# Kernel optimization log

Hardware: AMD Instinct MI355X
Metric: run time of the kernel (lower is better)

Reference implementation:

```python
import jax, jax.numpy as jnp
import numpy as np

IN_F = 2048
OUT_F = 2048
BS = 64  # block_size
NIB = IN_F // BS   # 32 in-blocks
NOB = OUT_F // BS  # 32 out-blocks


def setup_inputs() -> dict:
    key = jax.random.key(0)
    k_x, k_s1, k_s2, k_m = jax.random.split(key, 4)
    bound = 1.0 / np.sqrt(BS)
    x = jax.random.normal(k_x, (4, 4096, IN_F), dtype=jnp.float32)
    stage1 = jax.random.uniform(k_s1, (NIB * BS, BS), minval=-bound, maxval=bound, dtype=jnp.float32)
    stage2 = jax.random.uniform(k_s2, (NOB * BS, BS), minval=-bound, maxval=bound, dtype=jnp.float32)
    mix_w = jax.random.normal(k_m, (NOB * BS, NIB * BS), dtype=jnp.float32) / np.sqrt(IN_F)
    return {"x": x, "stage1": stage1, "stage2": stage2, "mix_w": mix_w}


def _blockdiag(x, weight, num_blocks):
    # x: [..., num_blocks*BS]; weight: [num_blocks*BS, BS] viewed as [g, c, d]
    shape = x.shape[:-1]
    xg = x.reshape(-1, num_blocks, BS)
    w = weight.reshape(num_blocks, BS, BS)
    y = jnp.einsum('ngc,gcd->ngd', xg, w)
    return y.reshape(*shape, num_blocks * BS)


def _shuffle(x):
    # interpret last dim as [BS, NIB], transpose to [NIB, BS]
    shape = x.shape[:-1]
    return x.reshape(-1, BS, NIB).transpose(0, 2, 1).reshape(*shape, NIB * BS)


def reference(x, stage1, stage2, mix_w):
    h = _blockdiag(x, stage1, NIB)          # [B,S,IN_F]
    h = _shuffle(h)                          # [B,S,IN_F]
    h = jnp.einsum('bsi,oi->bso', h, mix_w)  # dense mix, no bias
    return _blockdiag(h, stage2, NOB)        # [B,S,OUT_F]
```

## Files before the change

kernel.cpp:

```cpp
#include <hip/hip_runtime.h>
#include <stdint.h>

#define IN_F 2048
#define OUT_F 2048
#define MTOK 16384

typedef __attribute__((ext_vector_type(8))) __bf16 bf16x8;
typedef __attribute__((ext_vector_type(4))) float f32x4;
typedef __attribute__((ext_vector_type(4))) unsigned short us4;
typedef __attribute__((ext_vector_type(8))) unsigned short us8;

typedef const __attribute__((address_space(1))) void g_void;
typedef __attribute__((address_space(3))) void l_void;

__device__ __forceinline__ void async16(void* lds, const void* g) {
    __builtin_amdgcn_global_load_lds((g_void*)(uintptr_t)g, (l_void*)(uintptr_t)lds, 16, 0, 0);
}

__device__ __forceinline__ unsigned short f2bf(float x) {
    union { float f; uint32_t u; } v; v.f = x;
    uint32_t r = v.u + 0x7fffu + ((v.u >> 16) & 1u);
    return (unsigned short)(r >> 16);
}

__global__ void k_permute_mixw(const float* __restrict__ W, unsigned short* __restrict__ Bp) {
    __shared__ float row[2112];
    const int t = threadIdx.x;
    const float* src = W + (size_t)blockIdx.x * IN_F;
#pragma unroll
    for (int q = 0; q < 2; ++q) {
        int id4 = q * 256 + t;
        float4 v = *(const float4*)(src + id4 * 4);
        int i = id4 * 4;
        int b = i + (i >> 5);
        row[b] = v.x; row[b + 1] = v.y; row[b + 2] = v.z; row[b + 3] = v.w;
    }
    __syncthreads();
    unsigned short* dst = Bp + (size_t)blockIdx.x * IN_F;
#pragma unroll
    for (int q = 0; q < 8; ++q) {
        int j = q * 256 + t;
        int i = ((j & 31) << 6) | (j >> 5);
        dst[j] = f2bf(row[i + (i >> 5)]);
    }
}

__global__ void k_transpose_stages(const float* __restrict__ s1, const float* __restrict__ s2,
                                   unsigned short* __restrict__ W1T, unsigned short* __restrict__ W2T) {
    __shared__ float tile[64 * 65];
    const int b = blockIdx.x;
    const float* src = (b < 32 ? s1 : s2) + (size_t)(b & 31) * 4096;
    unsigned short* dst = (b < 32 ? W1T : W2T) + (size_t)(b & 31) * 4096;
    const int t = threadIdx.x;
#pragma unroll
    for (int q = 0; q < 16; ++q) {
        int id = q * 256 + t;
        tile[(id >> 6) * 65 + (id & 63)] = src[id];
    }
    __syncthreads();
#pragma unroll
    for (int q = 0; q < 16; ++q) {
        int id = q * 256 + t;
        int d = id >> 6, c = id & 63;
        dst[id] = f2bf(tile[c * 65 + d]);
    }
}

#define XS_LD 72
__global__ __launch_bounds__(256, 2) void k_stage1(
    const float* __restrict__ X, const unsigned short* __restrict__ W1T,
    unsigned short* __restrict__ H) {
    __shared__ unsigned short Xs[128 * XS_LD];
    __shared__ unsigned short Ws[64 * XS_LD];
    const int t = threadIdx.x;
    const int lane = t & 63, wave = t >> 6;
    const int quad = lane >> 4, l16 = lane & 15;
    const int m0 = blockIdx.x * 128;
    const int g = blockIdx.y;

    const unsigned short* Wg = W1T + g * 4096;
#pragma unroll
    for (int p = 0; p < 2; ++p) {
        int id = p * 256 + t;
        int r = id >> 3, c = id & 7;
        us8 v = *(const us8*)(Wg + r * 64 + c * 8);
        *(us8*)(Ws + r * XS_LD + c * 8) = v;
    }

    const float* Xg = X + (size_t)m0 * IN_F + g * 64;
#pragma unroll
    for (int q = 0; q < 8; ++q) {
        int id = q * 256 + t;
        int r = id >> 4, c4 = id & 15;
        float4 v = *(const float4*)(Xg + (size_t)r * IN_F + c4 * 4);
        us4 b; b.x = f2bf(v.x); b.y = f2bf(v.y); b.z = f2bf(v.z); b.w = f2bf(v.w);
        *(us4*)(Xs + r * XS_LD + c4 * 4) = b;
    }
    __syncthreads();

    f32x4 acc[2][4];
#pragma unroll
    for (int i = 0; i < 2; ++i)
#pragma unroll
        for (int j = 0; j < 4; ++j) acc[i][j] = (f32x4)0.f;

#pragma unroll
    for (int ks = 0; ks < 2; ++ks) {
        bf16x8 af[2], bfr[4];
#pragma unroll
        for (int i = 0; i < 2; ++i)
            af[i] = *(const bf16x8*)(Xs + (wave * 32 + i * 16 + l16) * XS_LD + ks * 32 + quad * 8);
#pragma unroll
        for (int j = 0; j < 4; ++j)
            bfr[j] = *(const bf16x8*)(Ws + (j * 16 + l16) * XS_LD + ks * 32 + quad * 8);
#pragma unroll
        for (int i = 0; i < 2; ++i)
#pragma unroll
            for (int j = 0; j < 4; ++j)
                acc[i][j] = __builtin_amdgcn_mfma_f32_16x16x32_bf16(af[i], bfr[j], acc[i][j], 0, 0, 0);
    }

    __syncthreads();
    unsigned short* Hs = Xs;
#pragma unroll
    for (int i = 0; i < 2; ++i)
#pragma unroll
        for (int j = 0; j < 4; ++j)
#pragma unroll
            for (int r = 0; r < 4; ++r)
                Hs[(wave * 32 + i * 16 + quad * 4 + r) * 64 + j * 16 + l16] = f2bf(acc[i][j][r]);
    __syncthreads();
#pragma unroll
    for (int p = 0; p < 4; ++p) {
        int id = p * 256 + t;
        int r = id >> 3, c = id & 7;
        us8 v = *(const us8*)(Hs + r * 64 + c * 8);
        *(us8*)(H + (size_t)(m0 + r) * IN_F + g * 64 + c * 8) = v;
    }
}

__global__ __launch_bounds__(256, 2) void k_mix_gemm(
    const unsigned short* __restrict__ A, const unsigned short* __restrict__ B,
    const unsigned short* __restrict__ W2T, float* __restrict__ C) {
    __shared__ unsigned short smem[16384];
    unsigned short* As = smem;
    unsigned short* Bs = smem + 8192;
    const int t = threadIdx.x;
    const int lane = t & 63, wave = t >> 6;
    const int quad = lane >> 4, l16 = lane & 15;
    const int mw = wave & 1, nw = wave >> 1;
    const int m0 = blockIdx.x * 128;
    const int n0 = blockIdx.y * 128;
    const int rr = t >> 3, chunk = t & 7;
    const int gsw = (chunk ^ (rr & 7)) * 8;
    const int lsw = l16 & 7;

    f32x4 acc[4][4];
#pragma unroll
    for (int i = 0; i < 4; ++i)
#pragma unroll
        for (int j = 0; j < 4; ++j) acc[i][j] = (f32x4)0.f;

    for (int kb = 0; kb < IN_F; kb += 64) {
#pragma unroll
        for (int q = 0; q < 4; ++q) {
            int r = q * 32 + rr;
            async16((char*)As + (size_t)(q * 4096 + t * 16),
                    A + (size_t)(m0 + r) * IN_F + kb + gsw);
            async16((char*)Bs + (size_t)(q * 4096 + t * 16),
                    B + (size_t)(n0 + r) * IN_F + kb + gsw);
        }
        __syncthreads();
#pragma unroll
        for (int ks = 0; ks < 2; ++ks) {
            bf16x8 af[4], bfr[4];
#pragma unroll
            for (int i = 0; i < 4; ++i)
                af[i] = *(const bf16x8*)(As + (mw * 64 + i * 16 + l16) * 64
                                            + (((ks * 4 + quad) ^ lsw) * 8));
#pragma unroll
            for (int j = 0; j < 4; ++j)
                bfr[j] = *(const bf16x8*)(Bs + (nw * 64 + j * 16 + l16) * 64
                                             + (((ks * 4 + quad) ^ lsw) * 8));
#pragma unroll
            for (int i = 0; i < 4; ++i)
#pragma unroll
                for (int j = 0; j < 4; ++j)
                    acc[i][j] = __builtin_amdgcn_mfma_f32_16x16x32_bf16(af[i], bfr[j], acc[i][j], 0, 0, 0);
        }
        __syncthreads();
    }

    unsigned short* P = smem + wave * 4096;
#pragma unroll
    for (int i = 0; i < 4; ++i)
#pragma unroll
        for (int j = 0; j < 4; ++j) {
            int cc = j * 2 + (l16 >> 3);
            int ci = l16 & 7;
#pragma unroll
            for (int r = 0; r < 4; ++r) {
                int pr = i * 16 + quad * 4 + r;
                P[pr * 64 + ((cc ^ (pr & 7)) * 8) + ci] = f2bf(acc[i][j][r]);
            }
        }

    const int g = (n0 >> 6) + nw;
    const unsigned short* W2g = W2T + g * 4096;
    bf16x8 wb[4][2];
#pragma unroll
    for (int j = 0; j < 4; ++j)
#pragma unroll
        for (int ks = 0; ks < 2; ++ks)
            wb[j][ks] = *(const bf16x8*)(W2g + (j * 16 + l16) * 64 + ks * 32 + quad * 8);

#pragma unroll
    for (int i = 0; i < 4; ++i) {
        bf16x8 pa0 = *(const bf16x8*)(P + (i * 16 + l16) * 64 + ((quad ^ lsw) * 8));
        bf16x8 pa1 = *(const bf16x8*)(P + (i * 16 + l16) * 64 + (((4 + quad) ^ lsw) * 8));
#pragma unroll
        for (int j = 0; j < 4; ++j) {
            f32x4 o = (f32x4)0.f;
            o = __builtin_amdgcn_mfma_f32_16x16x32_bf16(pa0, wb[j][0], o, 0, 0, 0);
            o = __builtin_amdgcn_mfma_f32_16x16x32_bf16(pa1, wb[j][1], o, 0, 0, 0);
            float* Cp = C + (size_t)(m0 + mw * 64 + i * 16 + quad * 4) * OUT_F
                          + (n0 + nw * 64 + j * 16 + l16);
#pragma unroll
            for (int r = 0; r < 4; ++r) Cp[(size_t)r * OUT_F] = o[r];
        }
    }
}

extern "C" void kernel_launch(void* const* d_in, const int* in_sizes, int n_in,
                              void* d_out, int out_size, void* d_ws, size_t ws_size,
                              hipStream_t stream) {
    const float* x  = (const float*)d_in[0];
    const float* s1 = (const float*)d_in[1];
    const float* s2 = (const float*)d_in[2];
    const float* mw = (const float*)d_in[3];
    float* out = (float*)d_out;

    char* ws = (char*)d_ws;
    unsigned short* hA  = (unsigned short*)ws;
    unsigned short* Bp  = (unsigned short*)(ws + (size_t)MTOK * IN_F * 2);
    unsigned short* W1T = (unsigned short*)(ws + (size_t)MTOK * IN_F * 2
                                               + (size_t)OUT_F * IN_F * 2);
    unsigned short* W2T = W1T + 32 * 4096;

    k_permute_mixw<<<2048, 256, 0, stream>>>(mw, Bp);
    k_transpose_stages<<<64, 256, 0, stream>>>(s1, s2, W1T, W2T);
    k_stage1<<<dim3(128, 32), 256, 0, stream>>>(x, W1T, hA);
    k_mix_gemm<<<dim3(128, 16), 256, 0, stream>>>(hA, Bp, W2T, out);
}
```

Baseline: 399.9 us.

## Merge prep kernels, load stage1 operands directly to registers, remap GEMM tiles

Fuses the mix-weight permute and the stage-weight transpose into one launch, which removes one kernel launch. Stage1 now loads X and W1T fragments straight into MFMA registers instead of staging them in LDS. That drops the input LDS buffers and one barrier, and lets the launch bound rise to 4 blocks per SM. The output staging buffer gets a padded stride. The mix GEMM reorders its block index so that consecutive blocks share the same A rows across all 16 N tiles, aiming for better L2 reuse of the activation tiles. The risk is uncoalesced strided global loads in stage1, since each lane reads 32 bytes from a different row.

```diff
diff --git a/kernel.cpp b/kernel.cpp
--- a/kernel.cpp
+++ b/kernel.cpp
@@ -23,55 +23,63 @@
     return (unsigned short)(r >> 16);
 }
 
-__global__ void k_permute_mixw(const float* __restrict__ W, unsigned short* __restrict__ Bp) {
-    __shared__ float row[2112];
+__device__ __forceinline__ bf16x8 f8_to_bf8(const float* __restrict__ p) {
+    float4 a = *(const float4*)p;
+    float4 b = *(const float4*)(p + 4);
+    union { us8 u; bf16x8 h; } r;
+    r.u[0] = f2bf(a.x); r.u[1] = f2bf(a.y); r.u[2] = f2bf(a.z); r.u[3] = f2bf(a.w);
+    r.u[4] = f2bf(b.x); r.u[5] = f2bf(b.y); r.u[6] = f2bf(b.z); r.u[7] = f2bf(b.w);
+    return r.h;
+}
+
+__global__ void k_prep(const float* __restrict__ W,
+                       const float* __restrict__ s1, const float* __restrict__ s2,
+                       unsigned short* __restrict__ Bp,
+                       unsigned short* __restrict__ W1T, unsigned short* __restrict__ W2T) {
+    __shared__ float buf[64 * 65];
     const int t = threadIdx.x;
-    const float* src = W + (size_t)blockIdx.x * IN_F;
-#pragma unroll
-    for (int q = 0; q < 2; ++q) {
-        int id4 = q * 256 + t;
-        float4 v = *(const float4*)(src + id4 * 4);
-        int i = id4 * 4;
-        int b = i + (i >> 5);
-        row[b] = v.x; row[b + 1] = v.y; row[b + 2] = v.z; row[b + 3] = v.w;
-    }
-    __syncthreads();
-    unsigned short* dst = Bp + (size_t)blockIdx.x * IN_F;
-#pragma unroll
-    for (int q = 0; q < 8; ++q) {
-        int j = q * 256 + t;
-        int i = ((j & 31) << 6) | (j >> 5);
-        dst[j] = f2bf(row[i + (i >> 5)]);
-    }
-}
-
-__global__ void k_transpose_stages(const float* __restrict__ s1, const float* __restrict__ s2,
-                                   unsigned short* __restrict__ W1T, unsigned short* __restrict__ W2T) {
-    __shared__ float tile[64 * 65];
-    const int b = blockIdx.x;
-    const float* src = (b < 32 ? s1 : s2) + (size_t)(b & 31) * 4096;
-    unsigned short* dst = (b < 32 ? W1T : W2T) + (size_t)(b & 31) * 4096;
-    const int t = threadIdx.x;
-#pragma unroll
-    for (int q = 0; q < 16; ++q) {
-        int id = q * 256 + t;
-        tile[(id >> 6) * 65 + (id & 63)] = src[id];
-    }
-    __syncthreads();
-#pragma unroll
-    for (int q = 0; q < 16; ++q) {
-        int id = q * 256 + t;
-        int d = id >> 6, c = id & 63;
-        dst[id] = f2bf(tile[c * 65 + d]);
-    }
-}
-
-#define XS_LD 72
-__global__ __launch_bounds__(256, 2) void k_stage1(
+    if (blockIdx.x < 2048) {
+        const float* src = W + (size_t)blockIdx.x * IN_F;
+#pragma unroll
+        for (int q = 0; q < 2; ++q) {
+            int id4 = q * 256 + t;
+            float4 v = *(const float4*)(src + id4 * 4);
+            int i = id4 * 4;
+            int b = i + (i >> 5);
+            buf[b] = v.x; buf[b + 1] = v.y; buf[b + 2] = v.z; buf[b + 3] = v.w;
+        }
+        __syncthreads();
+        unsigned short* dst = Bp + (size_t)blockIdx.x * IN_F;
+#pragma unroll
+        for (int q = 0; q < 8; ++q) {
+            int j = q * 256 + t;
+            int i = ((j & 31) << 6) | (j >> 5);
+            dst[j] = f2bf(buf[i + (i >> 5)]);
+        }
+    } else {
+        const int b = blockIdx.x - 2048;
+        const float* src = (b < 32 ? s1 : s2) + (size_t)(b & 31) * 4096;
+        unsigned short* dst = (b < 32 ? W1T : W2T) + (size_t)(b & 31) * 4096;
+#pragma unroll
+        for (int q = 0; q < 16; ++q) {
+            int id = q * 256 + t;
+            buf[(id >> 6) * 65 + (id & 63)] = src[id];
+        }
+        __syncthreads();
+#pragma unroll
+        for (int q = 0; q < 16; ++q) {
+            int id = q * 256 + t;
+            int d = id >> 6, c = id & 63;
+            dst[id] = f2bf(buf[c * 65 + d]);
+        }
+    }
+}
+
+#define HS_LD 72
+__global__ __launch_bounds__(256, 4) void k_stage1(
     const float* __restrict__ X, const unsigned short* __restrict__ W1T,
     unsigned short* __restrict__ H) {
-    __shared__ unsigned short Xs[128 * XS_LD];
-    __shared__ unsigned short Ws[64 * XS_LD];
+    __shared__ unsigned short Hs[128 * HS_LD];
     const int t = threadIdx.x;
     const int lane = t & 63, wave = t >> 6;
     const int quad = lane >> 4, l16 = lane & 15;
@@ -79,24 +87,20 @@
     const int g = blockIdx.y;
 
     const unsigned short* Wg = W1T + g * 4096;
-#pragma unroll
-    for (int p = 0; p < 2; ++p) {
-        int id = p * 256 + t;
-        int r = id >> 3, c = id & 7;
-        us8 v = *(const us8*)(Wg + r * 64 + c * 8);
-        *(us8*)(Ws + r * XS_LD + c * 8) = v;
-    }
-
-    const float* Xg = X + (size_t)m0 * IN_F + g * 64;
-#pragma unroll
-    for (int q = 0; q < 8; ++q) {
-        int id = q * 256 + t;
-        int r = id >> 4, c4 = id & 15;
-        float4 v = *(const float4*)(Xg + (size_t)r * IN_F + c4 * 4);
-        us4 b; b.x = f2bf(v.x); b.y = f2bf(v.y); b.z = f2bf(v.z); b.w = f2bf(v.w);
-        *(us4*)(Xs + r * XS_LD + c4 * 4) = b;
-    }
-    __syncthreads();
+    bf16x8 wf[4][2];
+#pragma unroll
+    for (int j = 0; j < 4; ++j)
+#pragma unroll
+        for (int ks = 0; ks < 2; ++ks)
+            wf[j][ks] = *(const bf16x8*)(Wg + (j * 16 + l16) * 64 + ks * 32 + quad * 8);
+
+    bf16x8 af[2][2];
+#pragma unroll
+    for (int i = 0; i < 2; ++i)
+#pragma unroll
+        for (int ks = 0; ks < 2; ++ks)
+            af[i][ks] = f8_to_bf8(X + (size_t)(m0 + wave * 32 + i * 16 + l16) * IN_F
+                                    + g * 64 + ks * 32 + quad * 8);
 
     f32x4 acc[2][4];
 #pragma unroll
@@ -105,36 +109,26 @@
         for (int j = 0; j < 4; ++j) acc[i][j] = (f32x4)0.f;
 
 #pragma unroll
-    for (int ks = 0; ks < 2; ++ks) {
-        bf16x8 af[2], bfr[4];
+    for (int ks = 0; ks < 2; ++ks)
 #pragma unroll
         for (int i = 0; i < 2; ++i)
-            af[i] = *(const bf16x8*)(Xs + (wave * 32 + i * 16 + l16) * XS_LD + ks * 32 + quad * 8);
+#pragma unroll
+            for (int j = 0; j < 4; ++j)
+                acc[i][j] = __builtin_amdgcn_mfma_f32_16x16x32_bf16(af[i][ks], wf[j][ks], acc[i][j], 0, 0, 0);
+
+#pragma unroll
+    for (int i = 0; i < 2; ++i)
 #pragma unroll
         for (int j = 0; j < 4; ++j)
-            bfr[j] = *(const bf16x8*)(Ws + (j * 16 + l16) * XS_LD + ks * 32 + quad * 8);
-#pragma unroll
-        for (int i = 0; i < 2; ++i)
-#pragma unroll
-            for (int j = 0; j < 4; ++j)
-                acc[i][j] = __builtin_amdgcn_mfma_f32_16x16x32_bf16(af[i], bfr[j], acc[i][j], 0, 0, 0);
-    }
-
-    __syncthreads();
-    unsigned short* Hs = Xs;
-#pragma unroll
-    for (int i = 0; i < 2; ++i)
-#pragma unroll
-        for (int j = 0; j < 4; ++j)
 #pragma unroll
             for (int r = 0; r < 4; ++r)
-                Hs[(wave * 32 + i * 16 + quad * 4 + r) * 64 + j * 16 + l16] = f2bf(acc[i][j][r]);
+                Hs[(wave * 32 + i * 16 + quad * 4 + r) * HS_LD + j * 16 + l16] = f2bf(acc[i][j][r]);
     __syncthreads();
 #pragma unroll
     for (int p = 0; p < 4; ++p) {
         int id = p * 256 + t;
         int r = id >> 3, c = id & 7;
-        us8 v = *(const us8*)(Hs + r * 64 + c * 8);
+        us8 v = *(const us8*)(Hs + r * HS_LD + c * 8);
         *(us8*)(H + (size_t)(m0 + r) * IN_F + g * 64 + c * 8) = v;
     }
 }
@@ -149,8 +143,9 @@
     const int lane = t & 63, wave = t >> 6;
     const int quad = lane >> 4, l16 = lane & 15;
     const int mw = wave & 1, nw = wave >> 1;
-    const int m0 = blockIdx.x * 128;
-    const int n0 = blockIdx.y * 128;
+    const int lin = blockIdx.y * 128 + blockIdx.x;
+    const int m0 = (lin >> 4) * 128;
+    const int n0 = (lin & 15) * 128;
     const int rr = t >> 3, chunk = t & 7;
     const int gsw = (chunk ^ (rr & 7)) * 8;
     const int lsw = l16 & 7;
@@ -247,8 +242,7 @@
                                                + (size_t)OUT_F * IN_F * 2);
     unsigned short* W2T = W1T + 32 * 4096;
 
-    k_permute_mixw<<<2048, 256, 0, stream>>>(mw, Bp);
-    k_transpose_stages<<<64, 256, 0, stream>>>(s1, s2, W1T, W2T);
+    k_prep<<<2112, 256, 0, stream>>>(mw, s1, s2, Bp, W1T, W2T);
     k_stage1<<<dim3(128, 32), 256, 0, stream>>>(x, W1T, hA);
     k_mix_gemm<<<dim3(128, 16), 256, 0, stream>>>(hA, Bp, W2T, out);
 }
```

New measurement: 393.0 us. Within noise of the previous version (-1.7%).
